# Kernel tuning notes

Hardware: AMD Instinct MI355X
Metric: run time of the kernel (lower is better)

Reference implementation:

```python
import jax, jax.numpy as jnp
import numpy as np

FEATURE_DIM = 256
NUM_HEADS = 8
HEAD_DIM = FEATURE_DIM // NUM_HEADS
LOCAL_RADIUS = 3.0
N_CUR = 4096
N_HIST = 4096
COORD_EXTENT = 16.0


def setup_inputs() -> dict:
    key = jax.random.key(0)
    ks = jax.random.split(key, 12)
    s = 1.0 / np.sqrt(FEATURE_DIM)  # ~nn.Linear init scale
    return {
        "current_feats": jax.random.normal(ks[0], (N_CUR, FEATURE_DIM), jnp.float32),
        "historical_feats": jax.random.normal(ks[1], (N_HIST, FEATURE_DIM), jnp.float32),
        "current_coords": jax.random.uniform(ks[2], (N_CUR, 3), jnp.float32) * COORD_EXTENT,
        "historical_coords": jax.random.uniform(ks[3], (N_HIST, 3), jnp.float32) * COORD_EXTENT,
        "Wq": jax.random.normal(ks[4], (FEATURE_DIM, FEATURE_DIM), jnp.float32) * s,
        "bq": jnp.zeros((FEATURE_DIM,), jnp.float32),
        "Wk": jax.random.normal(ks[5], (FEATURE_DIM, FEATURE_DIM), jnp.float32) * s,
        "bk": jnp.zeros((FEATURE_DIM,), jnp.float32),
        "Wv": jax.random.normal(ks[6], (FEATURE_DIM, FEATURE_DIM), jnp.float32) * s,
        "bv": jnp.zeros((FEATURE_DIM,), jnp.float32),
        "Wo": jax.random.normal(ks[7], (FEATURE_DIM, FEATURE_DIM), jnp.float32) * s,
        "bo": jnp.zeros((FEATURE_DIM,), jnp.float32),
    }


def reference(current_feats, historical_feats, current_coords, historical_coords,
              Wq, bq, Wk, bk, Wv, bv, Wo, bo):
    # local mask: squared distance <= radius^2 (identical to norm <= radius)
    diff = current_coords[:, None, :] - historical_coords[None, :, :]  # [Nq, Nk, 3]
    local_mask = jnp.sum(diff * diff, axis=-1) <= LOCAL_RADIUS ** 2      # [Nq, Nk]

    q = (current_feats @ Wq.T + bq).reshape(N_CUR, NUM_HEADS, HEAD_DIM)
    k = (historical_feats @ Wk.T + bk).reshape(N_HIST, NUM_HEADS, HEAD_DIM)
    v = (historical_feats @ Wv.T + bv).reshape(N_HIST, NUM_HEADS, HEAD_DIM)

    scores = jnp.einsum('qhd,khd->qhk', q, k) / np.sqrt(HEAD_DIM)        # [Nq, H, Nk]
    scores = jnp.where(local_mask[:, None, :], scores, -jnp.inf)
    attn = jax.nn.softmax(scores, axis=-1)  # dropout is identity in eval
    out = jnp.einsum('qhk,khd->qhd', attn, v).reshape(N_CUR, FEATURE_DIM)
    return out @ Wo.T + bo
```

## Files before the change

kernel.cpp:

```cpp
#include <hip/hip_runtime.h>
#include <math.h>

#define FDIM 256
#define NH 8
#define HD 32
#define NQ 4096
#define NKEY 4096
#define CAP 512
#define R2 9.0f

typedef _Float16 half8 __attribute__((ext_vector_type(8)));
typedef _Float16 half4v __attribute__((ext_vector_type(4)));
typedef float f32x4 __attribute__((ext_vector_type(4)));
typedef unsigned short ushort_t;

#define CB_CUR  0
#define CB_HIST 1048576
#define CB_WQ   2097152
#define CB_WK   2162688
#define CB_WV   2228224
#define CB_WO   2293760
#define CB_F4_TOTAL 589824

__global__ __launch_bounds__(256) void cast_all(const float* __restrict__ cur,
                                                const float* __restrict__ hist,
                                                const float* __restrict__ Wq,
                                                const float* __restrict__ Wk,
                                                const float* __restrict__ Wv,
                                                const float* __restrict__ Wo,
                                                _Float16* __restrict__ dst) {
    const int stride = gridDim.x * blockDim.x;
    for (int i4 = blockIdx.x * blockDim.x + threadIdx.x; i4 < CB_F4_TOTAL; i4 += stride) {
        const float* src;
        int base;
        if (i4 < 262144)      { src = cur;  base = 0; }
        else if (i4 < 524288) { src = hist; base = 262144; }
        else if (i4 < 540672) { src = Wq;   base = 524288; }
        else if (i4 < 557056) { src = Wk;   base = 540672; }
        else if (i4 < 573440) { src = Wv;   base = 557056; }
        else                  { src = Wo;   base = 573440; }
        float4 v = ((const float4*)src)[i4 - base];
        half4v h;
        h[0] = (_Float16)v.x; h[1] = (_Float16)v.y;
        h[2] = (_Float16)v.z; h[3] = (_Float16)v.w;
        ((half4v*)dst)[i4] = h;
    }
}

__device__ __forceinline__ void mfma_tile_16x64(const _Float16* __restrict__ A,
                                                const _Float16* __restrict__ W,
                                                int m0, int n0, int wave, int lane,
                                                f32x4 acc[4]) {
    const int row  = lane & 15;
    const int quad = lane >> 4;
    const _Float16* aptr = A + (size_t)(m0 + wave * 16 + row) * 256 + quad * 8;
    const _Float16* wptr = W + (size_t)(n0 + row) * 256 + quad * 8;
#pragma unroll
    for (int i = 0; i < 4; ++i) acc[i] = (f32x4){0.f, 0.f, 0.f, 0.f};
#pragma unroll
    for (int k0 = 0; k0 < 8; ++k0) {
        half8 a = *(const half8*)(aptr + k0 * 32);
#pragma unroll
        for (int nt = 0; nt < 4; ++nt) {
            half8 b = *(const half8*)(wptr + (size_t)nt * 16 * 256 + k0 * 32);
            acc[nt] = __builtin_amdgcn_mfma_f32_16x16x32_f16(a, b, acc[nt], 0, 0, 0);
        }
    }
}

__global__ __launch_bounds__(256) void qkv_mfma(const _Float16* __restrict__ cb,
                                                const float* __restrict__ bq,
                                                const float* __restrict__ bk,
                                                const float* __restrict__ bv,
                                                float* __restrict__ Qout,
                                                _Float16* __restrict__ KV) {
    const int z    = blockIdx.z;
    const int wave = threadIdx.x >> 6;
    const int lane = threadIdx.x & 63;
    const int m0   = blockIdx.y * 64;
    const int n0   = blockIdx.x * 64;

    const _Float16* A = (z == 0) ? (cb + CB_CUR) : (cb + CB_HIST);
    const _Float16* W = (z == 0) ? (cb + CB_WQ) : (z == 1) ? (cb + CB_WK) : (cb + CB_WV);
    const float* bias = (z == 0) ? bq : (z == 1) ? bk : bv;

    f32x4 acc[4];
    mfma_tile_16x64(A, W, m0, n0, wave, lane, acc);

    const int col  = lane & 15;
    const int quad = lane >> 4;
    float bs[4];
#pragma unroll
    for (int nt = 0; nt < 4; ++nt) bs[nt] = bias[n0 + nt * 16 + col];

    if (z == 0) {
#pragma unroll
        for (int nt = 0; nt < 4; ++nt)
#pragma unroll
            for (int r = 0; r < 4; ++r)
                Qout[(size_t)(m0 + wave * 16 + quad * 4 + r) * 256 + n0 + nt * 16 + col] =
                    acc[nt][r] + bs[nt];
    } else {
        const int off = (z == 1) ? 0 : 256;
#pragma unroll
        for (int nt = 0; nt < 4; ++nt)
#pragma unroll
            for (int r = 0; r < 4; ++r)
                KV[(size_t)(m0 + wave * 16 + quad * 4 + r) * 512 + off + n0 + nt * 16 + col] =
                    (_Float16)(acc[nt][r] + bs[nt]);
    }
}

__global__ __launch_bounds__(256) void o_mfma(const _Float16* __restrict__ Ob,
                                              const _Float16* __restrict__ Wo,
                                              const float* __restrict__ bo,
                                              float* __restrict__ out) {
    const int wave = threadIdx.x >> 6;
    const int lane = threadIdx.x & 63;
    const int m0   = blockIdx.y * 64;
    const int n0   = blockIdx.x * 64;

    f32x4 acc[4];
    mfma_tile_16x64(Ob, Wo, m0, n0, wave, lane, acc);

    const int col  = lane & 15;
    const int quad = lane >> 4;
#pragma unroll
    for (int nt = 0; nt < 4; ++nt) {
        const float b = bo[n0 + nt * 16 + col];
#pragma unroll
        for (int r = 0; r < 4; ++r)
            out[(size_t)(m0 + wave * 16 + quad * 4 + r) * 256 + n0 + nt * 16 + col] =
                acc[nt][r] + b;
    }
}

__global__ __launch_bounds__(256) void build_nbr(const float* __restrict__ qc,
                                                 const float* __restrict__ kc,
                                                 ushort_t* __restrict__ nbr,
                                                 int* __restrict__ cnt) {
    const int q    = blockIdx.x * 4 + (threadIdx.x >> 6);
    const int lane = threadIdx.x & 63;
    const float qx = qc[q * 3 + 0];
    const float qy = qc[q * 3 + 1];
    const float qz = qc[q * 3 + 2];
    int base = 0;
    for (int k0 = 0; k0 < NKEY; k0 += 64) {
        const int k = k0 + lane;
        float dx = __fsub_rn(qx, kc[k * 3 + 0]);
        float dy = __fsub_rn(qy, kc[k * 3 + 1]);
        float dz = __fsub_rn(qz, kc[k * 3 + 2]);
        float d2 = __fadd_rn(__fadd_rn(__fmul_rn(dx, dx), __fmul_rn(dy, dy)),
                             __fmul_rn(dz, dz));
        bool valid = (d2 <= R2);
        unsigned long long bal = __ballot(valid);
        if (valid) {
            int pos = base + __popcll(bal & ((1ull << lane) - 1ull));
            if (pos < CAP) nbr[(size_t)q * CAP + pos] = (ushort_t)k;
        }
        base += __popcll(bal);
    }
    if (lane == 0) cnt[q] = (base > CAP) ? CAP : base;
}

__global__ __launch_bounds__(256) void sparse_attn3(const float* __restrict__ Q,
                                                    const _Float16* __restrict__ KV,
                                                    const ushort_t* __restrict__ nbr,
                                                    const int* __restrict__ cnt,
                                                    _Float16* __restrict__ Ob) {
    const int q    = blockIdx.x * 4 + (threadIdx.x >> 6);
    const int lane = threadIdx.x & 63;
    const int p    = lane >> 5;
    const int h    = (lane >> 2) & 7;
    const int s    = lane & 3;

    const float* qrow = Q + (size_t)q * FDIM + h * HD + s * 8;
    float qv[8];
    {
        float4 a = *(const float4*)(qrow);
        float4 b = *(const float4*)(qrow + 4);
        qv[0] = a.x; qv[1] = a.y; qv[2] = a.z; qv[3] = a.w;
        qv[4] = b.x; qv[5] = b.y; qv[6] = b.z; qv[7] = b.w;
#pragma unroll
        for (int i = 0; i < 8; ++i) qv[i] *= 0.17677669529663687f;
    }

    float oA[8], oB[8];
#pragma unroll
    for (int i = 0; i < 8; ++i) { oA[i] = 0.f; oB[i] = 0.f; }
    float mA = -3e38f, lA = 0.f;
    float mB = -3e38f, lB = 0.f;

    const int n = cnt[q];
    const ushort_t* nl = nbr + (size_t)q * CAP;
    const int koff = h * HD + s * 8;

    for (int j = 0; j < n; j += 4) {
        const int  jA = j + p;
        const int  jB = j + 2 + p;
        const bool liveA = (jA < n);
        const bool liveB = (jB < n);
        const int  kA = nl[liveA ? jA : 0];
        const int  kB = nl[liveB ? jB : 0];
        const _Float16* rowA = KV + (size_t)kA * 512 + koff;
        const _Float16* rowB = KV + (size_t)kB * 512 + koff;
        half8 k8A = *(const half8*)(rowA);
        half8 v8A = *(const half8*)(rowA + 256);
        half8 k8B = *(const half8*)(rowB);
        half8 v8B = *(const half8*)(rowB + 256);

        float pa = 0.f, pb = 0.f;
#pragma unroll
        for (int i = 0; i < 8; ++i) {
            pa = fmaf(qv[i], (float)k8A[i], pa);
            pb = fmaf(qv[i], (float)k8B[i], pb);
        }
        pa += __shfl_xor(pa, 1, 64); pa += __shfl_xor(pa, 2, 64);
        pb += __shfl_xor(pb, 1, 64); pb += __shfl_xor(pb, 2, 64);

        const float scA = liveA ? pa : -INFINITY;
        const float scB = liveB ? pb : -INFINITY;

        const float nmA = fmaxf(mA, scA);
        const float sfA = __expf(mA - nmA);
        const float pwA = __expf(scA - nmA);
        lA = lA * sfA + pwA;
#pragma unroll
        for (int i = 0; i < 8; ++i)
            oA[i] = oA[i] * sfA + pwA * (float)v8A[i];
        mA = nmA;

        const float nmB = fmaxf(mB, scB);
        const float sfB = __expf(mB - nmB);
        const float pwB = __expf(scB - nmB);
        lB = lB * sfB + pwB;
#pragma unroll
        for (int i = 0; i < 8; ++i)
            oB[i] = oB[i] * sfB + pwB * (float)v8B[i];
        mB = nmB;
    }

    float m = fmaxf(mA, mB);
    const float sA = __expf(mA - m), sB = __expf(mB - m);
    float l = lA * sA + lB * sB;
    float o[8];
#pragma unroll
    for (int i = 0; i < 8; ++i) o[i] = oA[i] * sA + oB[i] * sB;

    const float gm  = fmaxf(m, __shfl_xor(m, 32, 64));
    const float sc2 = __expf(m - gm);
    l *= sc2;
#pragma unroll
    for (int i = 0; i < 8; ++i) o[i] *= sc2;
    l += __shfl_xor(l, 32, 64);
#pragma unroll
    for (int i = 0; i < 8; ++i) o[i] += __shfl_xor(o[i], 32, 64);

    if (p == 0) {
        const float inv = 1.0f / l;
        half8 ho;
#pragma unroll
        for (int i = 0; i < 8; ++i) ho[i] = (_Float16)(o[i] * inv);
        *(half8*)(Ob + (size_t)q * FDIM + h * HD + s * 8) = ho;
    }
}

extern "C" void kernel_launch(void* const* d_in, const int* in_sizes, int n_in,
                              void* d_out, int out_size, void* d_ws, size_t ws_size,
                              hipStream_t stream) {
    const float* cur_feats   = (const float*)d_in[0];
    const float* hist_feats  = (const float*)d_in[1];
    const float* cur_coords  = (const float*)d_in[2];
    const float* hist_coords = (const float*)d_in[3];
    const float* bq = (const float*)d_in[5];
    const float* bk = (const float*)d_in[7];
    const float* bv = (const float*)d_in[9];
    const float* bo = (const float*)d_in[11];
    float* out = (float*)d_out;

    char* w = (char*)d_ws;
    float*     Qb   = (float*)(w);
    _Float16*  KV   = (_Float16*)(w + (4 << 20));
    ushort_t*  nbr  = (ushort_t*)(w + (8 << 20));
    int*       cnt  = (int*)(w + (12 << 20));
    _Float16*  Ob   = (_Float16*)(w + (12 << 20) + (64 << 10));
    _Float16*  cb   = (_Float16*)(w + (15 << 20));

    cast_all<<<1024, 256, 0, stream>>>(cur_feats, hist_feats,
                                       (const float*)d_in[4], (const float*)d_in[6],
                                       (const float*)d_in[8], (const float*)d_in[10], cb);

    build_nbr<<<NQ / 4, 256, 0, stream>>>(cur_coords, hist_coords, nbr, cnt);

    qkv_mfma<<<dim3(4, 64, 3), 256, 0, stream>>>(cb, bq, bk, bv, Qb, KV);

    sparse_attn3<<<NQ / 4, 256, 0, stream>>>(Qb, KV, nbr, cnt, Ob);

    o_mfma<<<dim3(4, 64), 256, 0, stream>>>(Ob, cb + CB_WO, bo, out);
}
```

Before: 157.1 us.

## Store K/V head-major and assign whole heads per lane in sparse attention

K and V are now written head-major, so each key's 32-dim K and V slices for one head sit in one contiguous 128-byte row. The attention kernel gives each lane a full head and strides over neighbors 8 lanes apart, which removes the per-key cross-lane dot-product shuffles and the A/B dual streams. It adds a final 3-step shuffle merge of the 32-float accumulators and roughly 64+ more registers per thread, which may lower occupancy.

```diff
diff --git a/kernel.cpp b/kernel.cpp
--- a/kernel.cpp
+++ b/kernel.cpp
@@ -73,7 +73,7 @@
                                                 const float* __restrict__ bk,
                                                 const float* __restrict__ bv,
                                                 float* __restrict__ Qout,
-                                                _Float16* __restrict__ KV) {
+                                                _Float16* __restrict__ KV2) {
     const int z    = blockIdx.z;
     const int wave = threadIdx.x >> 6;
     const int lane = threadIdx.x & 63;
@@ -101,13 +101,19 @@
                 Qout[(size_t)(m0 + wave * 16 + quad * 4 + r) * 256 + n0 + nt * 16 + col] =
                     acc[nt][r] + bs[nt];
     } else {
-        const int off = (z == 1) ? 0 : 256;
-#pragma unroll
-        for (int nt = 0; nt < 4; ++nt)
-#pragma unroll
-            for (int r = 0; r < 4; ++r)
-                KV[(size_t)(m0 + wave * 16 + quad * 4 + r) * 512 + off + n0 + nt * 16 + col] =
+        const int zoff = (z == 1) ? 0 : 32;
+#pragma unroll
+        for (int nt = 0; nt < 4; ++nt) {
+            const int n  = n0 + nt * 16 + col;
+            const int hh = n >> 5;
+            const int d  = n & 31;
+#pragma unroll
+            for (int r = 0; r < 4; ++r) {
+                const int k = m0 + wave * 16 + quad * 4 + r;
+                KV2[(((size_t)hh * NKEY + k) << 6) + zoff + d] =
                     (_Float16)(acc[nt][r] + bs[nt]);
+            }
+        }
     }
 }
 
@@ -163,105 +169,100 @@
     if (lane == 0) cnt[q] = (base > CAP) ? CAP : base;
 }
 
-__global__ __launch_bounds__(256) void sparse_attn3(const float* __restrict__ Q,
-                                                    const _Float16* __restrict__ KV,
+__global__ __launch_bounds__(256) void sparse_attn4(const float* __restrict__ Q,
+                                                    const _Float16* __restrict__ KV2,
                                                     const ushort_t* __restrict__ nbr,
                                                     const int* __restrict__ cnt,
                                                     _Float16* __restrict__ Ob) {
     const int q    = blockIdx.x * 4 + (threadIdx.x >> 6);
     const int lane = threadIdx.x & 63;
-    const int p    = lane >> 5;
-    const int h    = (lane >> 2) & 7;
-    const int s    = lane & 3;
-
-    const float* qrow = Q + (size_t)q * FDIM + h * HD + s * 8;
-    float qv[8];
+    const int h    = lane >> 3;
+    const int j0   = lane & 7;
+
+    float qv[32];
     {
-        float4 a = *(const float4*)(qrow);
-        float4 b = *(const float4*)(qrow + 4);
-        qv[0] = a.x; qv[1] = a.y; qv[2] = a.z; qv[3] = a.w;
-        qv[4] = b.x; qv[5] = b.y; qv[6] = b.z; qv[7] = b.w;
-#pragma unroll
-        for (int i = 0; i < 8; ++i) qv[i] *= 0.17677669529663687f;
-    }
-
-    float oA[8], oB[8];
-#pragma unroll
-    for (int i = 0; i < 8; ++i) { oA[i] = 0.f; oB[i] = 0.f; }
-    float mA = -3e38f, lA = 0.f;
-    float mB = -3e38f, lB = 0.f;
+        const float* qrow = Q + (size_t)q * FDIM + h * HD;
+#pragma unroll
+        for (int i = 0; i < 8; ++i) {
+            float4 t = ((const float4*)qrow)[i];
+            qv[i * 4 + 0] = t.x * 0.17677669529663687f;
+            qv[i * 4 + 1] = t.y * 0.17677669529663687f;
+            qv[i * 4 + 2] = t.z * 0.17677669529663687f;
+            qv[i * 4 + 3] = t.w * 0.17677669529663687f;
+        }
+    }
+
+    float o[32];
+#pragma unroll
+    for (int i = 0; i < 32; ++i) o[i] = 0.f;
+    float m = -3e38f, l = 0.f;
 
     const int n = cnt[q];
     const ushort_t* nl = nbr + (size_t)q * CAP;
-    const int koff = h * HD + s * 8;
-
-    for (int j = 0; j < n; j += 4) {
-        const int  jA = j + p;
-        const int  jB = j + 2 + p;
-        const bool liveA = (jA < n);
-        const bool liveB = (jB < n);
-        const int  kA = nl[liveA ? jA : 0];
-        const int  kB = nl[liveB ? jB : 0];
-        const _Float16* rowA = KV + (size_t)kA * 512 + koff;
-        const _Float16* rowB = KV + (size_t)kB * 512 + koff;
-        half8 k8A = *(const half8*)(rowA);
-        half8 v8A = *(const half8*)(rowA + 256);
-        half8 k8B = *(const half8*)(rowB);
-        half8 v8B = *(const half8*)(rowB + 256);
-
-        float pa = 0.f, pb = 0.f;
+    const _Float16* hb = KV2 + ((size_t)h * NKEY << 6);
+
+    for (int j = j0; j < n; j += 8) {
+        const int k = nl[j];
+        const _Float16* r = hb + ((size_t)k << 6);
+        half8 k0v = ((const half8*)r)[0];
+        half8 k1v = ((const half8*)r)[1];
+        half8 k2v = ((const half8*)r)[2];
+        half8 k3v = ((const half8*)r)[3];
+        half8 v0v = ((const half8*)r)[4];
+        half8 v1v = ((const half8*)r)[5];
+        half8 v2v = ((const half8*)r)[6];
+        half8 v3v = ((const half8*)r)[7];
+
+        float p0 = 0.f, p1 = 0.f, p2 = 0.f, p3 = 0.f;
 #pragma unroll
         for (int i = 0; i < 8; ++i) {
-            pa = fmaf(qv[i], (float)k8A[i], pa);
-            pb = fmaf(qv[i], (float)k8B[i], pb);
-        }
-        pa += __shfl_xor(pa, 1, 64); pa += __shfl_xor(pa, 2, 64);
-        pb += __shfl_xor(pb, 1, 64); pb += __shfl_xor(pb, 2, 64);
-
-        const float scA = liveA ? pa : -INFINITY;
-        const float scB = liveB ? pb : -INFINITY;
-
-        const float nmA = fmaxf(mA, scA);
-        const float sfA = __expf(mA - nmA);
-        const float pwA = __expf(scA - nmA);
-        lA = lA * sfA + pwA;
-#pragma unroll
-        for (int i = 0; i < 8; ++i)
-            oA[i] = oA[i] * sfA + pwA * (float)v8A[i];
-        mA = nmA;
-
-        const float nmB = fmaxf(mB, scB);
-        const float sfB = __expf(mB - nmB);
-        const float pwB = __expf(scB - nmB);
-        lB = lB * sfB + pwB;
-#pragma unroll
-        for (int i = 0; i < 8; ++i)
-            oB[i] = oB[i] * sfB + pwB * (float)v8B[i];
-        mB = nmB;
-    }
-
-    float m = fmaxf(mA, mB);
-    const float sA = __expf(mA - m), sB = __expf(mB - m);
-    float l = lA * sA + lB * sB;
-    float o[8];
-#pragma unroll
-    for (int i = 0; i < 8; ++i) o[i] = oA[i] * sA + oB[i] * sB;
-
-    const float gm  = fmaxf(m, __shfl_xor(m, 32, 64));
-    const float sc2 = __expf(m - gm);
-    l *= sc2;
-#pragma unroll
-    for (int i = 0; i < 8; ++i) o[i] *= sc2;
-    l += __shfl_xor(l, 32, 64);
-#pragma unroll
-    for (int i = 0; i < 8; ++i) o[i] += __shfl_xor(o[i], 32, 64);
-
-    if (p == 0) {
+            p0 = fmaf(qv[i],      (float)k0v[i], p0);
+            p1 = fmaf(qv[8 + i],  (float)k1v[i], p1);
+            p2 = fmaf(qv[16 + i], (float)k2v[i], p2);
+            p3 = fmaf(qv[24 + i], (float)k3v[i], p3);
+        }
+        const float sc = (p0 + p1) + (p2 + p3);
+
+        const float nm = fmaxf(m, sc);
+        const float sf = __expf(m - nm);
+        const float pw = __expf(sc - nm);
+        l = l * sf + pw;
+#pragma unroll
+        for (int i = 0; i < 8; ++i) {
+            o[i]      = o[i]      * sf + pw * (float)v0v[i];
+            o[8 + i]  = o[8 + i]  * sf + pw * (float)v1v[i];
+            o[16 + i] = o[16 + i] * sf + pw * (float)v2v[i];
+            o[24 + i] = o[24 + i] * sf + pw * (float)v3v[i];
+        }
+        m = nm;
+    }
+
+#pragma unroll
+    for (int d = 1; d < 8; d <<= 1) {
+        const float m2 = __shfl_xor(m, d, 64);
+        const float l2 = __shfl_xor(l, d, 64);
+        const float nm = fmaxf(m, m2);
+        const float a  = __expf(m - nm);
+        const float b  = __expf(m2 - nm);
+        l = l * a + l2 * b;
+#pragma unroll
+        for (int i = 0; i < 32; ++i) {
+            const float o2 = __shfl_xor(o[i], d, 64);
+            o[i] = o[i] * a + o2 * b;
+        }
+        m = nm;
+    }
+
+    if (j0 == 0) {
         const float inv = 1.0f / l;
-        half8 ho;
-#pragma unroll
-        for (int i = 0; i < 8; ++i) ho[i] = (_Float16)(o[i] * inv);
-        *(half8*)(Ob + (size_t)q * FDIM + h * HD + s * 8) = ho;
+        _Float16* orow = Ob + (size_t)q * FDIM + h * HD;
+#pragma unroll
+        for (int w8 = 0; w8 < 4; ++w8) {
+            half8 ho;
+#pragma unroll
+            for (int i = 0; i < 8; ++i) ho[i] = (_Float16)(o[w8 * 8 + i] * inv);
+            ((half8*)orow)[w8] = ho;
+        }
     }
 }
 
@@ -280,7 +281,7 @@
 
     char* w = (char*)d_ws;
     float*     Qb   = (float*)(w);
-    _Float16*  KV   = (_Float16*)(w + (4 << 20));
+    _Float16*  KV2  = (_Float16*)(w + (4 << 20));
     ushort_t*  nbr  = (ushort_t*)(w + (8 << 20));
     int*       cnt  = (int*)(w + (12 << 20));
     _Float16*  Ob   = (_Float16*)(w + (12 << 20) + (64 << 10));
@@ -292,9 +293,9 @@
 
     build_nbr<<<NQ / 4, 256, 0, stream>>>(cur_coords, hist_coords, nbr, cnt);
 
-    qkv_mfma<<<dim3(4, 64, 3), 256, 0, stream>>>(cb, bq, bk, bv, Qb, KV);
-
-    sparse_attn3<<<NQ / 4, 256, 0, stream>>>(Qb, KV, nbr, cnt, Ob);
+    qkv_mfma<<<dim3(4, 64, 3), 256, 0, stream>>>(cb, bq, bk, bv, Qb, KV2);
+
+    sparse_attn4<<<NQ / 4, 256, 0, stream>>>(Qb, KV2, nbr, cnt, Ob);
 
     o_mfma<<<dim3(4, 64), 256, 0, stream>>>(Ob, cb + CB_WO, bo, out);
 }
```

New measurement: 176.5 us. 12.3% more time.

## Fuse cast and neighbor build; split each query's attention across four waves

Applied to the files above, without the earlier changes.

Merges the fp16 cast kernel and the neighbor-list build into one launch, with block ranges dispatching to each role, which removes a launch and lets the two independent jobs run concurrently. Sparse attention now assigns one block of four waves per query instead of one wave per query. Each wave processes a strided subset of neighbors with a single online-softmax stream, and the per-wave partial results are merged through shared memory. This adds parallelism and latency hiding for the gather-bound loop, at the cost of a block-level sync and a shared-memory reduction.

```diff
diff --git a/kernel.cpp b/kernel.cpp
--- a/kernel.cpp
+++ b/kernel.cpp
@@ -22,28 +22,58 @@
 #define CB_WO   2293760
 #define CB_F4_TOTAL 589824
 
-__global__ __launch_bounds__(256) void cast_all(const float* __restrict__ cur,
-                                                const float* __restrict__ hist,
-                                                const float* __restrict__ Wq,
-                                                const float* __restrict__ Wk,
-                                                const float* __restrict__ Wv,
-                                                const float* __restrict__ Wo,
-                                                _Float16* __restrict__ dst) {
-    const int stride = gridDim.x * blockDim.x;
-    for (int i4 = blockIdx.x * blockDim.x + threadIdx.x; i4 < CB_F4_TOTAL; i4 += stride) {
-        const float* src;
-        int base;
-        if (i4 < 262144)      { src = cur;  base = 0; }
-        else if (i4 < 524288) { src = hist; base = 262144; }
-        else if (i4 < 540672) { src = Wq;   base = 524288; }
-        else if (i4 < 557056) { src = Wk;   base = 540672; }
-        else if (i4 < 573440) { src = Wv;   base = 557056; }
-        else                  { src = Wo;   base = 573440; }
-        float4 v = ((const float4*)src)[i4 - base];
-        half4v h;
-        h[0] = (_Float16)v.x; h[1] = (_Float16)v.y;
-        h[2] = (_Float16)v.z; h[3] = (_Float16)v.w;
-        ((half4v*)dst)[i4] = h;
+__global__ __launch_bounds__(256) void prep(const float* __restrict__ cur,
+                                            const float* __restrict__ hist,
+                                            const float* __restrict__ Wq,
+                                            const float* __restrict__ Wk,
+                                            const float* __restrict__ Wv,
+                                            const float* __restrict__ Wo,
+                                            _Float16* __restrict__ dst,
+                                            const float* __restrict__ qc,
+                                            const float* __restrict__ kc,
+                                            ushort_t* __restrict__ nbr,
+                                            int* __restrict__ cnt) {
+    if (blockIdx.x < 1024) {
+        const int q    = blockIdx.x * 4 + (threadIdx.x >> 6);
+        const int lane = threadIdx.x & 63;
+        const float qx = qc[q * 3 + 0];
+        const float qy = qc[q * 3 + 1];
+        const float qz = qc[q * 3 + 2];
+        int base = 0;
+        for (int k0 = 0; k0 < NKEY; k0 += 64) {
+            const int k = k0 + lane;
+            float dx = __fsub_rn(qx, kc[k * 3 + 0]);
+            float dy = __fsub_rn(qy, kc[k * 3 + 1]);
+            float dz = __fsub_rn(qz, kc[k * 3 + 2]);
+            float d2 = __fadd_rn(__fadd_rn(__fmul_rn(dx, dx), __fmul_rn(dy, dy)),
+                                 __fmul_rn(dz, dz));
+            bool valid = (d2 <= R2);
+            unsigned long long bal = __ballot(valid);
+            if (valid) {
+                int pos = base + __popcll(bal & ((1ull << lane) - 1ull));
+                if (pos < CAP) nbr[(size_t)q * CAP + pos] = (ushort_t)k;
+            }
+            base += __popcll(bal);
+        }
+        if (lane == 0) cnt[q] = (base > CAP) ? CAP : base;
+    } else {
+        const int stride = 1024 * 256;
+        for (int i4 = (blockIdx.x - 1024) * 256 + threadIdx.x; i4 < CB_F4_TOTAL;
+             i4 += stride) {
+            const float* src;
+            int base;
+            if (i4 < 262144)      { src = cur;  base = 0; }
+            else if (i4 < 524288) { src = hist; base = 262144; }
+            else if (i4 < 540672) { src = Wq;   base = 524288; }
+            else if (i4 < 557056) { src = Wk;   base = 540672; }
+            else if (i4 < 573440) { src = Wv;   base = 557056; }
+            else                  { src = Wo;   base = 573440; }
+            float4 v = ((const float4*)src)[i4 - base];
+            half4v h;
+            h[0] = (_Float16)v.x; h[1] = (_Float16)v.y;
+            h[2] = (_Float16)v.z; h[3] = (_Float16)v.w;
+            ((half4v*)dst)[i4] = h;
+        }
     }
 }
 
@@ -135,133 +165,109 @@
     }
 }
 
-__global__ __launch_bounds__(256) void build_nbr(const float* __restrict__ qc,
-                                                 const float* __restrict__ kc,
-                                                 ushort_t* __restrict__ nbr,
-                                                 int* __restrict__ cnt) {
-    const int q    = blockIdx.x * 4 + (threadIdx.x >> 6);
-    const int lane = threadIdx.x & 63;
-    const float qx = qc[q * 3 + 0];
-    const float qy = qc[q * 3 + 1];
-    const float qz = qc[q * 3 + 2];
-    int base = 0;
-    for (int k0 = 0; k0 < NKEY; k0 += 64) {
-        const int k = k0 + lane;
-        float dx = __fsub_rn(qx, kc[k * 3 + 0]);
-        float dy = __fsub_rn(qy, kc[k * 3 + 1]);
-        float dz = __fsub_rn(qz, kc[k * 3 + 2]);
-        float d2 = __fadd_rn(__fadd_rn(__fmul_rn(dx, dx), __fmul_rn(dy, dy)),
-                             __fmul_rn(dz, dz));
-        bool valid = (d2 <= R2);
-        unsigned long long bal = __ballot(valid);
-        if (valid) {
-            int pos = base + __popcll(bal & ((1ull << lane) - 1ull));
-            if (pos < CAP) nbr[(size_t)q * CAP + pos] = (ushort_t)k;
-        }
-        base += __popcll(bal);
-    }
-    if (lane == 0) cnt[q] = (base > CAP) ? CAP : base;
-}
-
-__global__ __launch_bounds__(256) void sparse_attn3(const float* __restrict__ Q,
+__global__ __launch_bounds__(256) void sparse_attn6(const float* __restrict__ Q,
                                                     const _Float16* __restrict__ KV,
                                                     const ushort_t* __restrict__ nbr,
                                                     const int* __restrict__ cnt,
                                                     _Float16* __restrict__ Ob) {
-    const int q    = blockIdx.x * 4 + (threadIdx.x >> 6);
-    const int lane = threadIdx.x & 63;
+    __shared__ float sm[4][32][12];
+    const int q    = blockIdx.x;
+    const int t    = threadIdx.x;
+    const int wave = t >> 6;
+    const int lane = t & 63;
     const int p    = lane >> 5;
     const int h    = (lane >> 2) & 7;
     const int s    = lane & 3;
 
-    const float* qrow = Q + (size_t)q * FDIM + h * HD + s * 8;
     float qv[8];
     {
-        float4 a = *(const float4*)(qrow);
-        float4 b = *(const float4*)(qrow + 4);
-        qv[0] = a.x; qv[1] = a.y; qv[2] = a.z; qv[3] = a.w;
-        qv[4] = b.x; qv[5] = b.y; qv[6] = b.z; qv[7] = b.w;
-#pragma unroll
-        for (int i = 0; i < 8; ++i) qv[i] *= 0.17677669529663687f;
-    }
-
-    float oA[8], oB[8];
-#pragma unroll
-    for (int i = 0; i < 8; ++i) { oA[i] = 0.f; oB[i] = 0.f; }
-    float mA = -3e38f, lA = 0.f;
-    float mB = -3e38f, lB = 0.f;
+        const float* qrow = Q + (size_t)q * FDIM + h * HD + s * 8;
+        float4 a = ((const float4*)qrow)[0];
+        float4 b = ((const float4*)qrow)[1];
+        const float sc = 0.17677669529663687f;
+        qv[0] = a.x * sc; qv[1] = a.y * sc; qv[2] = a.z * sc; qv[3] = a.w * sc;
+        qv[4] = b.x * sc; qv[5] = b.y * sc; qv[6] = b.z * sc; qv[7] = b.w * sc;
+    }
+
+    float o[8];
+#pragma unroll
+    for (int i = 0; i < 8; ++i) o[i] = 0.f;
+    float m = -3e38f, l = 0.f;
 
     const int n = cnt[q];
     const ushort_t* nl = nbr + (size_t)q * CAP;
     const int koff = h * HD + s * 8;
 
-    for (int j = 0; j < n; j += 4) {
-        const int  jA = j + p;
-        const int  jB = j + 2 + p;
-        const bool liveA = (jA < n);
-        const bool liveB = (jB < n);
-        const int  kA = nl[liveA ? jA : 0];
-        const int  kB = nl[liveB ? jB : 0];
-        const _Float16* rowA = KV + (size_t)kA * 512 + koff;
-        const _Float16* rowB = KV + (size_t)kB * 512 + koff;
-        half8 k8A = *(const half8*)(rowA);
-        half8 v8A = *(const half8*)(rowA + 256);
-        half8 k8B = *(const half8*)(rowB);
-        half8 v8B = *(const half8*)(rowB + 256);
-
-        float pa = 0.f, pb = 0.f;
+    for (int j = 2 * wave + p; j < n; j += 8) {
+        const int k = nl[j];
+        const _Float16* r = KV + ((size_t)k << 9) + koff;
+        half8 k8 = *(const half8*)(r);
+        half8 v8 = *(const half8*)(r + 256);
+
+        float part = 0.f;
+#pragma unroll
+        for (int i = 0; i < 8; ++i)
+            part = fmaf(qv[i], (float)k8[i], part);
+        part += __shfl_xor(part, 1, 64);
+        part += __shfl_xor(part, 2, 64);
+
+        const float nm = fmaxf(m, part);
+        const float sf = __expf(m - nm);
+        const float pw = __expf(part - nm);
+        l = l * sf + pw;
+#pragma unroll
+        for (int i = 0; i < 8; ++i)
+            o[i] = o[i] * sf + pw * (float)v8[i];
+        m = nm;
+    }
+
+    {
+        const float m2 = __shfl_xor(m, 32, 64);
+        const float l2 = __shfl_xor(l, 32, 64);
+        const float nm = fmaxf(m, m2);
+        const float a  = __expf(m - nm);
+        const float b  = __expf(m2 - nm);
+        l = l * a + l2 * b;
 #pragma unroll
         for (int i = 0; i < 8; ++i) {
-            pa = fmaf(qv[i], (float)k8A[i], pa);
-            pb = fmaf(qv[i], (float)k8B[i], pb);
-        }
-        pa += __shfl_xor(pa, 1, 64); pa += __shfl_xor(pa, 2, 64);
-        pb += __shfl_xor(pb, 1, 64); pb += __shfl_xor(pb, 2, 64);
-
-        const float scA = liveA ? pa : -INFINITY;
-        const float scB = liveB ? pb : -INFINITY;
-
-        const float nmA = fmaxf(mA, scA);
-        const float sfA = __expf(mA - nmA);
-        const float pwA = __expf(scA - nmA);
-        lA = lA * sfA + pwA;
-#pragma unroll
-        for (int i = 0; i < 8; ++i)
-            oA[i] = oA[i] * sfA + pwA * (float)v8A[i];
-        mA = nmA;
-
-        const float nmB = fmaxf(mB, scB);
-        const float sfB = __expf(mB - nmB);
-        const float pwB = __expf(scB - nmB);
-        lB = lB * sfB + pwB;
-#pragma unroll
-        for (int i = 0; i < 8; ++i)
-            oB[i] = oB[i] * sfB + pwB * (float)v8B[i];
-        mB = nmB;
-    }
-
-    float m = fmaxf(mA, mB);
-    const float sA = __expf(mA - m), sB = __expf(mB - m);
-    float l = lA * sA + lB * sB;
-    float o[8];
-#pragma unroll
-    for (int i = 0; i < 8; ++i) o[i] = oA[i] * sA + oB[i] * sB;
-
-    const float gm  = fmaxf(m, __shfl_xor(m, 32, 64));
-    const float sc2 = __expf(m - gm);
-    l *= sc2;
-#pragma unroll
-    for (int i = 0; i < 8; ++i) o[i] *= sc2;
-    l += __shfl_xor(l, 32, 64);
-#pragma unroll
-    for (int i = 0; i < 8; ++i) o[i] += __shfl_xor(o[i], 32, 64);
-
-    if (p == 0) {
-        const float inv = 1.0f / l;
+            const float o2 = __shfl_xor(o[i], 32, 64);
+            o[i] = o[i] * a + o2 * b;
+        }
+        m = nm;
+    }
+
+    if (lane < 32) {
+        float* dst = &sm[wave][lane][0];
+        *(float4*)(dst)     = (float4){o[0], o[1], o[2], o[3]};
+        *(float4*)(dst + 4) = (float4){o[4], o[5], o[6], o[7]};
+        dst[8] = m; dst[9] = l;
+    }
+    __syncthreads();
+
+    if (t < 32) {
+        float4 x0 = *(const float4*)&sm[0][t][0];
+        float4 x1 = *(const float4*)&sm[0][t][4];
+        float O[8] = {x0.x, x0.y, x0.z, x0.w, x1.x, x1.y, x1.z, x1.w};
+        float M = sm[0][t][8], L = sm[0][t][9];
+#pragma unroll
+        for (int w = 1; w < 4; ++w) {
+            float4 y0 = *(const float4*)&sm[w][t][0];
+            float4 y1 = *(const float4*)&sm[w][t][4];
+            const float m2 = sm[w][t][8], l2 = sm[w][t][9];
+            const float nm = fmaxf(M, m2);
+            const float a  = __expf(M - nm);
+            const float b  = __expf(m2 - nm);
+            L = L * a + l2 * b;
+            float y[8] = {y0.x, y0.y, y0.z, y0.w, y1.x, y1.y, y1.z, y1.w};
+#pragma unroll
+            for (int i = 0; i < 8; ++i) O[i] = O[i] * a + y[i] * b;
+            M = nm;
+        }
+        const float inv = 1.0f / L;
         half8 ho;
 #pragma unroll
-        for (int i = 0; i < 8; ++i) ho[i] = (_Float16)(o[i] * inv);
-        *(half8*)(Ob + (size_t)q * FDIM + h * HD + s * 8) = ho;
+        for (int i = 0; i < 8; ++i) ho[i] = (_Float16)(O[i] * inv);
+        *(half8*)(Ob + (size_t)q * FDIM + t * 8) = ho;
     }
 }
 
@@ -286,15 +292,14 @@
     _Float16*  Ob   = (_Float16*)(w + (12 << 20) + (64 << 10));
     _Float16*  cb   = (_Float16*)(w + (15 << 20));
 
-    cast_all<<<1024, 256, 0, stream>>>(cur_feats, hist_feats,
-                                       (const float*)d_in[4], (const float*)d_in[6],
-                                       (const float*)d_in[8], (const float*)d_in[10], cb);
-
-    build_nbr<<<NQ / 4, 256, 0, stream>>>(cur_coords, hist_coords, nbr, cnt);
+    prep<<<2048, 256, 0, stream>>>(cur_feats, hist_feats,
+                                   (const float*)d_in[4], (const float*)d_in[6],
+                                   (const float*)d_in[8], (const float*)d_in[10], cb,
+                                   cur_coords, hist_coords, nbr, cnt);
 
     qkv_mfma<<<dim3(4, 64, 3), 256, 0, stream>>>(cb, bq, bk, bv, Qb, KV);
 
-    sparse_attn3<<<NQ / 4, 256, 0, stream>>>(Qb, KV, nbr, cnt, Ob);
+    sparse_attn6<<<NQ, 256, 0, stream>>>(Qb, KV, nbr, cnt, Ob);
 
     o_mfma<<<dim3(4, 64), 256, 0, stream>>>(Ob, cb + CB_WO, bo, out);
 }
```

Result: faster. 150.1 us (-4.5%).
